# Kernel optimization log

Measured on AMD Instinct MI355X. Metric: run time of the kernel, lower is better.

The kernel has to match this reference:

```python
import jax, jax.numpy as jnp
import numpy as np

L, DIN, D, NL = 16384, 256, 768, 8
EPS = 1e-5


def _ln(x, g, b):
    mu = jnp.mean(x, axis=-1, keepdims=True)
    var = jnp.mean(jnp.square(x - mu), axis=-1, keepdims=True)
    return (x - mu) * jax.lax.rsqrt(var + EPS) * g + b


def setup_inputs() -> dict:
    key = jax.random.key(0)
    ks = iter(jax.random.split(key, 24))
    nrm = lambda shape, s=0.02: jax.random.normal(next(ks), shape, jnp.float32) * s
    return {
        "node_features": jax.random.normal(next(ks), (L, DIN), jnp.float32),
        "W_proj": nrm((DIN, D)), "b_proj": jnp.zeros((D,), jnp.float32),
        "ln_s_g": jnp.ones((NL, D), jnp.float32), "ln_s_b": jnp.zeros((NL, D), jnp.float32),
        "W_in": nrm((NL, D, D)), "b_in": jnp.zeros((NL, D), jnp.float32),
        "W_gate": nrm((NL, D, D)), "b_gate": jnp.zeros((NL, D), jnp.float32),
        "W_out": nrm((NL, D, D)), "b_out": jnp.zeros((NL, D), jnp.float32),
        "decay_logit": nrm((NL, D), 0.5),
        "ln_f_g": jnp.ones((NL, D), jnp.float32), "ln_f_b": jnp.zeros((NL, D), jnp.float32),
        "W_ff1": nrm((NL, D, 2 * D)), "b_ff1": jnp.zeros((NL, 2 * D), jnp.float32),
        "W_ff2": nrm((NL, 2 * D, D)), "b_ff2": jnp.zeros((NL, D), jnp.float32),
        "ln_o_g": jnp.ones((D,), jnp.float32), "ln_o_b": jnp.zeros((D,), jnp.float32),
    }


def reference(node_features, W_proj, b_proj, ln_s_g, ln_s_b, W_in, b_in,
              W_gate, b_gate, W_out, b_out, decay_logit, ln_f_g, ln_f_b,
              W_ff1, b_ff1, W_ff2, b_ff2, ln_o_g, ln_o_b):
    x = node_features @ W_proj + b_proj  # [L, D]
    for l in range(NL):
        h = _ln(x, ln_s_g[l], ln_s_b[l])
        u = h @ W_in[l] + b_in[l]                      # [L, D]
        gate = jax.nn.sigmoid(h @ W_gate[l] + b_gate[l])
        decay = jax.nn.sigmoid(decay_logit[l])         # [D]

        def step(state, u_t):
            state = decay * state + u_t
            return state, state

        _, states = jax.lax.scan(step, jnp.zeros((D,), x.dtype), u)  # [L, D]
        x = x + (states * gate) @ W_out[l] + b_out[l]
        hf = _ln(x, ln_f_g[l], ln_f_b[l])
        x = x + jax.nn.silu(hf @ W_ff1[l] + b_ff1[l]) @ W_ff2[l] + b_ff2[l]
    return _ln(x, ln_o_g, ln_o_b)
```

## Files before the change

### kernel.cpp

```cpp
#include <hip/hip_runtime.h>
#include <hip/hip_bf16.h>
#include <math.h>
#include <string.h>

#define L_TOK 16384
#define D_INP 256
#define D_MOD 768
#define D_FF  1536
#define N_LAYER 8
#define S_T 64
#define S_G 256
#define EPSV 1e-5f

typedef short bf16x8 __attribute__((ext_vector_type(8)));
typedef float f32x4 __attribute__((ext_vector_type(4)));
typedef __hip_bfloat16 bf16;
typedef unsigned int u32;
typedef unsigned short u16;

__device__ __forceinline__ float fsigmoid(float z) { return 1.0f / (1.0f + __expf(-z)); }

__device__ __forceinline__ u16 f2bf(float f) {
  __hip_bfloat16 h = __float2bfloat16(f);
  u16 r; memcpy(&r, &h, 2); return r;
}
__device__ __forceinline__ float bf2f(u16 v) {
  u32 x = ((u32)v) << 16; float f; memcpy(&f, &x, 4); return f;
}

__device__ __forceinline__ void glds16(const short* g, short* l) {
  __builtin_amdgcn_global_load_lds(
      (const __attribute__((address_space(1))) unsigned int*)(g),
      (__attribute__((address_space(3))) unsigned int*)(l), 16, 0, 0);
}

__global__ void k_f32_to_bf16v(const float4* __restrict__ src, ushort4* __restrict__ dst, int n4) {
  int i = blockIdx.x * blockDim.x + threadIdx.x;
  if (i < n4) {
    float4 v = src[i];
    ushort4 o; o.x = f2bf(v.x); o.y = f2bf(v.y); o.z = f2bf(v.z); o.w = f2bf(v.w);
    dst[i] = o;
  }
}

template<bool FOLD>
__global__ void k_transpose_fold(const float* __restrict__ src, bf16* __restrict__ dst,
                                 int R, int C, size_t sstride, size_t dstride,
                                 const float* __restrict__ gv, const float* __restrict__ bv,
                                 float* __restrict__ wacc, float* __restrict__ bacc,
                                 int vstride) {
  __shared__ float tile[32][33];
  int z = blockIdx.z;
  const float* s = src + (size_t)z * sstride;
  bf16* d = dst + (size_t)z * dstride;
  int r0 = blockIdx.y * 32, c0 = blockIdx.x * 32;
  int tx = threadIdx.x, ty = threadIdx.y;
#pragma unroll
  for (int i = ty; i < 32; i += 8)
    tile[i][tx] = s[(size_t)(r0 + i) * C + (c0 + tx)];
  __syncthreads();
  float gk = 1.0f;
  if (FOLD) gk = gv[(size_t)z * R + r0 + tx];
#pragma unroll
  for (int i = ty; i < 32; i += 8) {
    float val = tile[tx][i];
    if (FOLD) val *= gk;
    d[(size_t)(c0 + i) * R + (r0 + tx)] = __float2bfloat16(val);
  }
  if (FOLD && ty == 0) {
    const float* gz = gv + (size_t)z * R + r0;
    const float* bz = bv + (size_t)z * R + r0;
    float s1 = 0.f, s2 = 0.f;
#pragma unroll 8
    for (int j = 0; j < 32; j++) {
      float wv = tile[j][tx];
      s1 += gz[j] * wv;
      s2 += bz[j] * wv;
    }
    atomicAdd(&wacc[(size_t)z * vstride + c0 + tx], s1);
    atomicAdd(&bacc[(size_t)z * vstride + c0 + tx], s2);
  }
}

template<int MODE, bool LNFOLD, bool STATS>
__global__ __launch_bounds__(256, 4) void k_gemm128(
    const short* __restrict__ A, const short* __restrict__ Bt,
    const float* __restrict__ bias, const float* __restrict__ bias2,
    const float* __restrict__ wvec, const float* __restrict__ bvec,
    const float* __restrict__ stats_in, float* __restrict__ stats_out,
    u16* __restrict__ res, u16* __restrict__ outp, u16* __restrict__ outp2,
    int N, int K, int ncol)
{
  __shared__ short As[2][128 * 32];
  __shared__ short Bs[2][128 * 32];
  __shared__ float s_mu[128], s_rv[128];
  const int tid = threadIdx.x;
  const int lane = tid & 63, w = tid >> 6;
  const int wr = w >> 1, wc = w & 1;
  const int l16 = lane & 15, qd = lane >> 4;

  const int b = blockIdx.x;
  const int xcd = b & 7, t = b >> 3;
  const int m0 = (xcd * 16 + t / ncol) * 128;
  const int n0 = (t % ncol) * 128;

  const int sr = lane >> 2, sc = lane & 3;
  const int ar = w * 32 + sr;
  const int acx = sc ^ ((ar >> 1) & 3);
  const short* ag0 = A  + (size_t)(m0 + ar) * K + acx * 8;
  const short* ag1 = ag0 + (size_t)16 * K;
  const short* bg0 = Bt + (size_t)(n0 + ar) * K + acx * 8;
  const short* bg1 = bg0 + (size_t)16 * K;

  const int fo = (qd ^ ((l16 >> 1) & 3)) * 8 + l16 * 32;

  f32x4 acc[4][4];
#pragma unroll
  for (int i = 0; i < 4; i++)
#pragma unroll
    for (int j = 0; j < 4; j++) acc[i][j] = (f32x4){0.f, 0.f, 0.f, 0.f};

  {
    short* a0 = &As[0][w * 1024];
    glds16(ag0, a0); glds16(ag1, a0 + 512);
    short* b0 = &Bs[0][w * 1024];
    glds16(bg0, b0); glds16(bg1, b0 + 512);
  }
  if (LNFOLD && tid < 128) {
    float sv  = stats_in[2 * (m0 + tid)];
    float sq  = stats_in[2 * (m0 + tid) + 1];
    float mu  = sv * (1.0f / (float)D_MOD);
    float var = sq * (1.0f / (float)D_MOD) - mu * mu;
    s_mu[tid] = mu;
    s_rv[tid] = 1.0f / sqrtf(var + EPSV);
  }
  int p = 0;
  for (int k0 = 0; k0 < K; k0 += 32, p ^= 1) {
    __syncthreads();
    if (k0 + 32 < K) {
      short* a0 = &As[p ^ 1][w * 1024];
      glds16(ag0 + k0 + 32, a0); glds16(ag1 + k0 + 32, a0 + 512);
      short* b0 = &Bs[p ^ 1][w * 1024];
      glds16(bg0 + k0 + 32, b0); glds16(bg1 + k0 + 32, b0 + 512);
    }
    const short* afb = &As[p][wr * 2048 + fo];
    const short* bfb = &Bs[p][wc * 2048 + fo];
    bf16x8 af[4], bfr[4];
#pragma unroll
    for (int rt = 0; rt < 4; rt++) af[rt] = *(const bf16x8*)(afb + rt * 512);
#pragma unroll
    for (int ct = 0; ct < 4; ct++) bfr[ct] = *(const bf16x8*)(bfb + ct * 512);
#pragma unroll
    for (int rt = 0; rt < 4; rt++)
#pragma unroll
      for (int ct = 0; ct < 4; ct++)
        acc[rt][ct] = __builtin_amdgcn_mfma_f32_16x16x32_bf16(af[rt], bfr[ct], acc[rt][ct], 0, 0, 0);
  }

  const float* bb = bias;
  u16* op = outp;
  int nofs = 0, Nout = N;
  bool sig = false;
  if (MODE == 4) {
    Nout = N >> 1;
    if (n0 >= Nout) { bb = bias2; op = outp2; nofs = Nout; sig = true; }
  }
  const int gmb = m0 + wr * 64 + qd * 4;
  const int gnb = n0 + wc * 64 + l16;
  float bc[4], wv4[4], bv4[4];
#pragma unroll
  for (int ct = 0; ct < 4; ct++) {
    int gn = gnb + ct * 16;
    bc[ct] = bb[gn - nofs];
    if (LNFOLD) { wv4[ct] = wvec[gn]; bv4[ct] = bvec[gn]; }
  }
#pragma unroll
  for (int rt = 0; rt < 4; rt++) {
#pragma unroll
    for (int r = 0; r < 4; r++) {
      const int gm = gmb + rt * 16 + r;
      float mu = 0.f, rv = 0.f;
      if (LNFOLD) { mu = s_mu[gm - m0]; rv = s_rv[gm - m0]; }
      float ps = 0.f, ps2 = 0.f;
#pragma unroll
      for (int ct = 0; ct < 4; ct++) {
        int gn = gnb + ct * 16;
        float vv = acc[rt][ct][r];
        if (LNFOLD) vv = rv * vv - rv * mu * wv4[ct] + bv4[ct] + bc[ct];
        else        vv += bc[ct];
        if (MODE == 2) vv = vv * fsigmoid(vv);
        if (MODE == 4 && sig) vv = fsigmoid(vv);
        size_t oidx = (size_t)gm * Nout + (gn - nofs);
        if (MODE == 3) vv += bf2f(res[oidx]);
        u16 rb = f2bf(vv);
        op[oidx] = rb;
        if (STATS) { float fv = bf2f(rb); ps += fv; ps2 += fv * fv; }
      }
      if (STATS) {
#pragma unroll
        for (int o = 1; o < 16; o <<= 1) {
          ps  += __shfl_xor(ps, o, 64);
          ps2 += __shfl_xor(ps2, o, 64);
        }
        if (l16 == 0) {
          atomicAdd(&stats_out[2 * gm], ps);
          atomicAdd(&stats_out[2 * gm + 1], ps2);
        }
      }
    }
  }
}

__global__ void k_scan_a(const bf16* __restrict__ u, const float* __restrict__ dl,
                         float* __restrict__ clast) {
  int t = threadIdx.x;
  int g = blockIdx.x;
  int d0 = t * 4;
  float dec[4], s[4] = {0.f, 0.f, 0.f, 0.f};
#pragma unroll
  for (int c = 0; c < 4; c++) dec[c] = fsigmoid(dl[d0 + c]);
  const ushort4* up = (const ushort4*)(u + (size_t)g * S_T * D_MOD) + t;
  for (int tt = 0; tt < S_T; tt++) {
    ushort4 uv = up[(size_t)tt * 192];
    s[0] = fmaf(dec[0], s[0], bf2f(uv.x));
    s[1] = fmaf(dec[1], s[1], bf2f(uv.y));
    s[2] = fmaf(dec[2], s[2], bf2f(uv.z));
    s[3] = fmaf(dec[3], s[3], bf2f(uv.w));
  }
#pragma unroll
  for (int c = 0; c < 4; c++) clast[(size_t)g * D_MOD + d0 + c] = s[c];
}

__global__ void k_scan_b(const float* __restrict__ clast, const float* __restrict__ dl,
                         float* __restrict__ carry) {
  int d = threadIdx.x;
  float decay = fsigmoid(dl[d]);
  float aT = decay;
#pragma unroll
  for (int i = 0; i < 6; i++) aT *= aT;
  float c = 0.f;
  for (int g = 0; g < S_G; g++) {
    carry[(size_t)g * D_MOD + d] = c;
    c = fmaf(aT, c, clast[(size_t)g * D_MOD + d]);
  }
}

__global__ void k_scan_c(const bf16* __restrict__ u, const float* __restrict__ dl,
                         const float* __restrict__ carry, bf16* __restrict__ gate_s) {
  int t = threadIdx.x;
  int g = blockIdx.x;
  int d0 = t * 4;
  float dec[4], s[4];
#pragma unroll
  for (int c = 0; c < 4; c++) {
    dec[c] = fsigmoid(dl[d0 + c]);
    s[c] = carry[(size_t)g * D_MOD + d0 + c];
  }
  const ushort4* up = (const ushort4*)(u + (size_t)g * S_T * D_MOD) + t;
  ushort4* gp = (ushort4*)(gate_s + (size_t)g * S_T * D_MOD) + t;
  for (int tt = 0; tt < S_T; tt++) {
    ushort4 uv = up[(size_t)tt * 192];
    ushort4 gv = gp[(size_t)tt * 192];
    s[0] = fmaf(dec[0], s[0], bf2f(uv.x));
    s[1] = fmaf(dec[1], s[1], bf2f(uv.y));
    s[2] = fmaf(dec[2], s[2], bf2f(uv.z));
    s[3] = fmaf(dec[3], s[3], bf2f(uv.w));
    ushort4 ov;
    ov.x = f2bf(s[0] * bf2f(gv.x));
    ov.y = f2bf(s[1] * bf2f(gv.y));
    ov.z = f2bf(s[2] * bf2f(gv.z));
    ov.w = f2bf(s[3] * bf2f(gv.w));
    gp[(size_t)tt * 192] = ov;
  }
}

__global__ __launch_bounds__(256) void k_ln_final(const u16* __restrict__ x,
    const float* __restrict__ stats, const float* __restrict__ g,
    const float* __restrict__ b, float* __restrict__ outp) {
  int wv = threadIdx.x >> 6, lane = threadIdx.x & 63;
  int row = blockIdx.x * 4 + wv;
  float sv = stats[2 * row], sq = stats[2 * row + 1];
  float mu = sv * (1.0f / (float)D_MOD);
  float var = sq * (1.0f / (float)D_MOD) - mu * mu;
  float rv = 1.0f / sqrtf(var + EPSV);
  const ushort4* xr = (const ushort4*)(x + (size_t)row * D_MOD);
  const float4* g4 = (const float4*)g;
  const float4* b4 = (const float4*)b;
  float4* o4 = (float4*)(outp + (size_t)row * D_MOD);
#pragma unroll
  for (int j = 0; j < 3; j++) {
    int f = j * 64 + lane;
    ushort4 xv = xr[f];
    float4 gg = g4[f], bb = b4[f], ov;
    ov.x = (bf2f(xv.x) - mu) * rv * gg.x + bb.x;
    ov.y = (bf2f(xv.y) - mu) * rv * gg.y + bb.y;
    ov.z = (bf2f(xv.z) - mu) * rv * gg.z + bb.z;
    ov.w = (bf2f(xv.w) - mu) * rv * gg.w + bb.w;
    o4[f] = ov;
  }
}

extern "C" void kernel_launch(void* const* d_in, const int* in_sizes, int n_in,
                              void* d_out, int out_size, void* d_ws, size_t ws_size,
                              hipStream_t stream) {
  const float* nf     = (const float*)d_in[0];
  const float* W_proj = (const float*)d_in[1];
  const float* b_proj = (const float*)d_in[2];
  const float* ln_s_g = (const float*)d_in[3];
  const float* ln_s_b = (const float*)d_in[4];
  const float* W_in   = (const float*)d_in[5];
  const float* b_in   = (const float*)d_in[6];
  const float* W_gate = (const float*)d_in[7];
  const float* b_gate = (const float*)d_in[8];
  const float* W_out  = (const float*)d_in[9];
  const float* b_out  = (const float*)d_in[10];
  const float* dlogit = (const float*)d_in[11];
  const float* ln_f_g = (const float*)d_in[12];
  const float* ln_f_b = (const float*)d_in[13];
  const float* W_ff1  = (const float*)d_in[14];
  const float* b_ff1  = (const float*)d_in[15];
  const float* W_ff2  = (const float*)d_in[16];
  const float* b_ff2  = (const float*)d_in[17];
  const float* ln_o_g = (const float*)d_in[18];
  const float* ln_o_b = (const float*)d_in[19];
  (void)in_sizes; (void)n_in;

  char* ws = (char*)d_ws;
  size_t off = 0;
  auto alloc = [&](size_t bytes) -> char* {
    char* p = ws + off;
    off = (off + bytes + 255) & ~(size_t)255;
    return p;
  };
  const bool big = ws_size >= (160ull << 20);
  const size_t wmul = big ? N_LAYER : 1;

  u16*   x     = (u16*)alloc(2ull * L_TOK * D_MOD);
  char*  ug    = alloc(2ull * L_TOK * D_FF);
  u16*   u     = (u16*)ug;
  u16*   gate  = (u16*)(ug + 2ull * L_TOK * D_MOD);
  u16*   tb    = (u16*)ug;
  u16*   nfb   = (u16*)ug;
  bf16*  WprojT= (bf16*)alloc(2ull * D_INP * D_MOD);
  bf16*  WigT  = (bf16*)alloc(2ull * wmul * (2 * D_MOD) * D_MOD);
  bf16*  WoT   = (bf16*)alloc(2ull * wmul * D_MOD * D_MOD);
  bf16*  Wff1T = (bf16*)alloc(2ull * wmul * D_MOD * D_FF);
  bf16*  Wff2T = (bf16*)alloc(2ull * wmul * D_FF * D_MOD);
  float* clast = (float*)alloc(sizeof(float) * (size_t)S_G * D_MOD);
  float* carry = (float*)alloc(sizeof(float) * (size_t)S_G * D_MOD);
  char*  zbase = alloc(0);
  float* stats = (float*)alloc(sizeof(float) * 17ull * L_TOK * 2);
  float* wvig  = (float*)alloc(sizeof(float) * N_LAYER * 2 * D_MOD);
  float* bvig  = (float*)alloc(sizeof(float) * N_LAYER * 2 * D_MOD);
  float* wvf1  = (float*)alloc(sizeof(float) * N_LAYER * D_FF);
  float* bvf1  = (float*)alloc(sizeof(float) * N_LAYER * D_FF);
  size_t zbytes = (size_t)((char*)ws + off - zbase);
  hipMemsetAsync(zbase, 0, zbytes, stream);

  const size_t DD = (size_t)D_MOD * D_MOD, DF = (size_t)D_MOD * D_FF;
  auto statslot = [&](int s) { return stats + (size_t)s * L_TOK * 2; };
  dim3 tb32(32, 8);
  k_f32_to_bf16v<<<(L_TOK * D_INP / 4 + 255) / 256, 256, 0, stream>>>(
      (const float4*)nf, (ushort4*)nfb, L_TOK * D_INP / 4);
  k_transpose_fold<false><<<dim3(D_MOD / 32, D_INP / 32, 1), tb32, 0, stream>>>(
      W_proj, WprojT, D_INP, D_MOD, 0, 0, nullptr, nullptr, nullptr, nullptr, 0);
  if (big) {
    k_transpose_fold<true><<<dim3(D_MOD / 32, D_MOD / 32, N_LAYER), tb32, 0, stream>>>(
        W_in,   WigT,      D_MOD, D_MOD, DD, 2 * DD, ln_s_g, ln_s_b, wvig,       bvig,       2 * D_MOD);
    k_transpose_fold<true><<<dim3(D_MOD / 32, D_MOD / 32, N_LAYER), tb32, 0, stream>>>(
        W_gate, WigT + DD, D_MOD, D_MOD, DD, 2 * DD, ln_s_g, ln_s_b, wvig + D_MOD, bvig + D_MOD, 2 * D_MOD);
    k_transpose_fold<false><<<dim3(D_MOD / 32, D_MOD / 32, N_LAYER), tb32, 0, stream>>>(
        W_out,  WoT,       D_MOD, D_MOD, DD, DD, nullptr, nullptr, nullptr, nullptr, 0);
    k_transpose_fold<true><<<dim3(D_FF / 32,  D_MOD / 32, N_LAYER), tb32, 0, stream>>>(
        W_ff1,  Wff1T,     D_MOD, D_FF,  DF, DF, ln_f_g, ln_f_b, wvf1, bvf1, D_FF);
    k_transpose_fold<false><<<dim3(D_MOD / 32, D_FF / 32,  N_LAYER), tb32, 0, stream>>>(
        W_ff2,  Wff2T,     D_FF,  D_MOD, DF, DF, nullptr, nullptr, nullptr, nullptr, 0);
  }

  k_gemm128<0, false, true><<<128 * 6, 256, 0, stream>>>(
      (const short*)nfb, (const short*)WprojT, b_proj, nullptr, nullptr, nullptr,
      nullptr, statslot(0), nullptr, x, nullptr, D_MOD, D_INP, 6);

  for (int l = 0; l < N_LAYER; l++) {
    const bf16 *wigT, *woT, *wf1T, *wf2T;
    if (big) {
      wigT = WigT  + (size_t)l * 2 * DD;
      woT  = WoT   + (size_t)l * DD;
      wf1T = Wff1T + (size_t)l * DF;
      wf2T = Wff2T + (size_t)l * DF;
    } else {
      k_transpose_fold<true><<<dim3(D_MOD / 32, D_MOD / 32, 1), tb32, 0, stream>>>(
          W_in + (size_t)l * DD, WigT, D_MOD, D_MOD, 0, 0,
          ln_s_g + l * D_MOD, ln_s_b + l * D_MOD, wvig + (size_t)l * 2 * D_MOD, bvig + (size_t)l * 2 * D_MOD, 0);
      k_transpose_fold<true><<<dim3(D_MOD / 32, D_MOD / 32, 1), tb32, 0, stream>>>(
          W_gate + (size_t)l * DD, WigT + DD, D_MOD, D_MOD, 0, 0,
          ln_s_g + l * D_MOD, ln_s_b + l * D_MOD, wvig + (size_t)l * 2 * D_MOD + D_MOD, bvig + (size_t)l * 2 * D_MOD + D_MOD, 0);
      k_transpose_fold<false><<<dim3(D_MOD / 32, D_MOD / 32, 1), tb32, 0, stream>>>(
          W_out + (size_t)l * DD, WoT, D_MOD, D_MOD, 0, 0, nullptr, nullptr, nullptr, nullptr, 0);
      k_transpose_fold<true><<<dim3(D_FF / 32, D_MOD / 32, 1), tb32, 0, stream>>>(
          W_ff1 + (size_t)l * DF, Wff1T, D_MOD, D_FF, 0, 0,
          ln_f_g + l * D_MOD, ln_f_b + l * D_MOD, wvf1 + (size_t)l * D_FF, bvf1 + (size_t)l * D_FF, 0);
      k_transpose_fold<false><<<dim3(D_MOD / 32, D_FF / 32, 1), tb32, 0, stream>>>(
          W_ff2 + (size_t)l * DF, Wff2T, D_FF, D_MOD, 0, 0, nullptr, nullptr, nullptr, nullptr, 0);
      wigT = WigT; woT = WoT; wf1T = Wff1T; wf2T = Wff2T;
    }

    k_gemm128<4, true, false><<<128 * 12, 256, 0, stream>>>(
        (const short*)x, (const short*)wigT, b_in + l * D_MOD, b_gate + l * D_MOD,
        wvig + (size_t)l * 2 * D_MOD, bvig + (size_t)l * 2 * D_MOD,
        statslot(2 * l), nullptr, nullptr, u, gate, 2 * D_MOD, D_MOD, 12);
    k_scan_a<<<S_G, 192, 0, stream>>>((const bf16*)u, dlogit + l * D_MOD, clast);
    k_scan_b<<<1, D_MOD, 0, stream>>>(clast, dlogit + l * D_MOD, carry);
    k_scan_c<<<S_G, 192, 0, stream>>>((const bf16*)u, dlogit + l * D_MOD, carry, (bf16*)gate);
    k_gemm128<3, false, true><<<128 * 6, 256, 0, stream>>>(
        (const short*)gate, (const short*)woT, b_out + l * D_MOD, nullptr, nullptr, nullptr,
        nullptr, statslot(2 * l + 1), x, x, nullptr, D_MOD, D_MOD, 6);
    k_gemm128<2, true, false><<<128 * 12, 256, 0, stream>>>(
        (const short*)x, (const short*)wf1T, b_ff1 + l * D_FF, nullptr,
        wvf1 + (size_t)l * D_FF, bvf1 + (size_t)l * D_FF,
        statslot(2 * l + 1), nullptr, nullptr, tb, nullptr, D_FF, D_MOD, 12);
    k_gemm128<3, false, true><<<128 * 6, 256, 0, stream>>>(
        (const short*)tb, (const short*)wf2T, b_ff2 + l * D_MOD, nullptr, nullptr, nullptr,
        nullptr, statslot(2 * l + 2), x, x, nullptr, D_MOD, D_FF, 6);
  }

  k_ln_final<<<L_TOK / 4, 256, 0, stream>>>(x, statslot(2 * N_LAYER), ln_o_g, ln_o_b, (float*)d_out);
}
```

Before: 2.277 ms.

## Process two M-tiles per GEMM block, add 64-wide N tiles, fuse scan phases

The GEMM kernel now has each block compute two consecutive 128-row tiles, prefetching the second tile's first K-slice while the first is still computing. All GEMMs launch 768 blocks, so the grid fits in a single wave. The N=768 GEMMs switch to 128x64 tiles so their block count matches the wider ones. The scan's carry pass is folded into the first scan kernel through a last-block-done atomic counter, removing one launch. The trade-offs are a serialized tail in each block and a single-block carry pass that runs after all other scan blocks finish.

```diff
diff --git a/kernel.cpp b/kernel.cpp
--- a/kernel.cpp
+++ b/kernel.cpp
@@ -82,8 +82,8 @@
   }
 }
 
-template<int MODE, bool LNFOLD, bool STATS>
-__global__ __launch_bounds__(256, 4) void k_gemm128(
+template<int MODE, bool LNFOLD, bool STATS, int BN>
+__global__ __launch_bounds__(256, 4) void k_gemm(
     const short* __restrict__ A, const short* __restrict__ Bt,
     const float* __restrict__ bias, const float* __restrict__ bias2,
     const float* __restrict__ wvec, const float* __restrict__ bvec,
@@ -91,128 +91,169 @@
     u16* __restrict__ res, u16* __restrict__ outp, u16* __restrict__ outp2,
     int N, int K, int ncol)
 {
+  constexpr int CT = BN / 32;
   __shared__ short As[2][128 * 32];
-  __shared__ short Bs[2][128 * 32];
+  __shared__ short Bs[2][BN * 32];
   __shared__ float s_mu[128], s_rv[128];
   const int tid = threadIdx.x;
   const int lane = tid & 63, w = tid >> 6;
   const int wr = w >> 1, wc = w & 1;
   const int l16 = lane & 15, qd = lane >> 4;
 
-  const int b = blockIdx.x;
-  const int xcd = b & 7, t = b >> 3;
-  const int m0 = (xcd * 16 + t / ncol) * 128;
-  const int n0 = (t % ncol) * 128;
-
   const int sr = lane >> 2, sc = lane & 3;
   const int ar = w * 32 + sr;
-  const int acx = sc ^ ((ar >> 1) & 3);
-  const short* ag0 = A  + (size_t)(m0 + ar) * K + acx * 8;
-  const short* ag1 = ag0 + (size_t)16 * K;
-  const short* bg0 = Bt + (size_t)(n0 + ar) * K + acx * 8;
-  const short* bg1 = bg0 + (size_t)16 * K;
+  const int acxA = sc ^ ((ar >> 1) & 3);
+  const int bn64 = w * 16 + (lane >> 2);
+  const int acxB = sc ^ ((bn64 >> 1) & 3);
+
+  const int bid = blockIdx.x;
+  const int xcd = bid & 7, q = bid >> 3;
+  const int ccol = q % ncol, r2 = q / ncol;
+  const short *pA0[2], *pA1[2], *pB0[2], *pB1[2];
+  int pm0[2], pn0[2];
+#pragma unroll
+  for (int t = 0; t < 2; t++) {
+    int m0 = (xcd * 16 + r2 * 2 + t) * 128;
+    int n0 = ccol * BN;
+    pm0[t] = m0; pn0[t] = n0;
+    pA0[t] = A + (size_t)(m0 + ar) * K + acxA * 8;
+    pA1[t] = pA0[t] + (size_t)16 * K;
+    if (BN == 128) {
+      pB0[t] = Bt + (size_t)(n0 + ar) * K + acxA * 8;
+      pB1[t] = pB0[t] + (size_t)16 * K;
+    } else {
+      pB0[t] = Bt + (size_t)(n0 + bn64) * K + acxB * 8;
+      pB1[t] = nullptr;
+    }
+  }
+
+  auto issue = [&](int t, int ko, int st) {
+    short* al = &As[st][w * 1024];
+    glds16(pA0[t] + ko, al); glds16(pA1[t] + ko, al + 512);
+    if (BN == 128) {
+      short* bl = &Bs[st][w * 1024];
+      glds16(pB0[t] + ko, bl); glds16(pB1[t] + ko, bl + 512);
+    } else {
+      short* bl = &Bs[st][w * 512];
+      glds16(pB0[t] + ko, bl);
+    }
+  };
 
   const int fo = (qd ^ ((l16 >> 1) & 3)) * 8 + l16 * 32;
 
-  f32x4 acc[4][4];
+  f32x4 acc[4][CT];
 #pragma unroll
   for (int i = 0; i < 4; i++)
 #pragma unroll
-    for (int j = 0; j < 4; j++) acc[i][j] = (f32x4){0.f, 0.f, 0.f, 0.f};
-
-  {
-    short* a0 = &As[0][w * 1024];
-    glds16(ag0, a0); glds16(ag1, a0 + 512);
-    short* b0 = &Bs[0][w * 1024];
-    glds16(bg0, b0); glds16(bg1, b0 + 512);
-  }
+    for (int j = 0; j < CT; j++) acc[i][j] = (f32x4){0.f, 0.f, 0.f, 0.f};
+
+  issue(0, 0, 0);
   if (LNFOLD && tid < 128) {
-    float sv  = stats_in[2 * (m0 + tid)];
-    float sq  = stats_in[2 * (m0 + tid) + 1];
+    float sv  = stats_in[2 * (pm0[0] + tid)];
+    float sq  = stats_in[2 * (pm0[0] + tid) + 1];
     float mu  = sv * (1.0f / (float)D_MOD);
     float var = sq * (1.0f / (float)D_MOD) - mu * mu;
     s_mu[tid] = mu;
     s_rv[tid] = 1.0f / sqrtf(var + EPSV);
   }
+
+  const int NI = K >> 5;
   int p = 0;
-  for (int k0 = 0; k0 < K; k0 += 32, p ^= 1) {
-    __syncthreads();
-    if (k0 + 32 < K) {
-      short* a0 = &As[p ^ 1][w * 1024];
-      glds16(ag0 + k0 + 32, a0); glds16(ag1 + k0 + 32, a0 + 512);
-      short* b0 = &Bs[p ^ 1][w * 1024];
-      glds16(bg0 + k0 + 32, b0); glds16(bg1 + k0 + 32, b0 + 512);
-    }
-    const short* afb = &As[p][wr * 2048 + fo];
-    const short* bfb = &Bs[p][wc * 2048 + fo];
-    bf16x8 af[4], bfr[4];
-#pragma unroll
-    for (int rt = 0; rt < 4; rt++) af[rt] = *(const bf16x8*)(afb + rt * 512);
-#pragma unroll
-    for (int ct = 0; ct < 4; ct++) bfr[ct] = *(const bf16x8*)(bfb + ct * 512);
-#pragma unroll
-    for (int rt = 0; rt < 4; rt++)
-#pragma unroll
-      for (int ct = 0; ct < 4; ct++)
-        acc[rt][ct] = __builtin_amdgcn_mfma_f32_16x16x32_bf16(af[rt], bfr[ct], acc[rt][ct], 0, 0, 0);
-  }
-
-  const float* bb = bias;
-  u16* op = outp;
-  int nofs = 0, Nout = N;
-  bool sig = false;
-  if (MODE == 4) {
-    Nout = N >> 1;
-    if (n0 >= Nout) { bb = bias2; op = outp2; nofs = Nout; sig = true; }
-  }
-  const int gmb = m0 + wr * 64 + qd * 4;
-  const int gnb = n0 + wc * 64 + l16;
-  float bc[4], wv4[4], bv4[4];
-#pragma unroll
-  for (int ct = 0; ct < 4; ct++) {
-    int gn = gnb + ct * 16;
-    bc[ct] = bb[gn - nofs];
-    if (LNFOLD) { wv4[ct] = wvec[gn]; bv4[ct] = bvec[gn]; }
-  }
-#pragma unroll
-  for (int rt = 0; rt < 4; rt++) {
-#pragma unroll
-    for (int r = 0; r < 4; r++) {
-      const int gm = gmb + rt * 16 + r;
-      float mu = 0.f, rv = 0.f;
-      if (LNFOLD) { mu = s_mu[gm - m0]; rv = s_rv[gm - m0]; }
-      float ps = 0.f, ps2 = 0.f;
-#pragma unroll
-      for (int ct = 0; ct < 4; ct++) {
+  for (int t = 0; t < 2; t++) {
+    for (int i = 0; i < NI; i++) {
+      __syncthreads();
+      if (LNFOLD && t == 1 && i == 0 && tid < 128) {
+        float sv  = stats_in[2 * (pm0[1] + tid)];
+        float sq  = stats_in[2 * (pm0[1] + tid) + 1];
+        float mu  = sv * (1.0f / (float)D_MOD);
+        float var = sq * (1.0f / (float)D_MOD) - mu * mu;
+        s_mu[tid] = mu;
+        s_rv[tid] = 1.0f / sqrtf(var + EPSV);
+      }
+      if (i + 1 < NI)      issue(t, (i + 1) << 5, p ^ 1);
+      else if (t == 0)     issue(1, 0, p ^ 1);
+      const short* afb = &As[p][wr * 2048 + fo];
+      const short* bfb = &Bs[p][wc * (BN / 2) * 32 + fo];
+      bf16x8 af[4], bfr[CT];
+#pragma unroll
+      for (int rt = 0; rt < 4; rt++) af[rt] = *(const bf16x8*)(afb + rt * 512);
+#pragma unroll
+      for (int ct = 0; ct < CT; ct++) bfr[ct] = *(const bf16x8*)(bfb + ct * 512);
+#pragma unroll
+      for (int rt = 0; rt < 4; rt++)
+#pragma unroll
+        for (int ct = 0; ct < CT; ct++)
+          acc[rt][ct] = __builtin_amdgcn_mfma_f32_16x16x32_bf16(af[rt], bfr[ct], acc[rt][ct], 0, 0, 0);
+      p ^= 1;
+    }
+
+    {
+      const int m0 = pm0[t], n0 = pn0[t];
+      const float* bb = bias;
+      u16* op = outp;
+      int nofs = 0, Nout = N;
+      bool sig = false;
+      if (MODE == 4) {
+        Nout = N >> 1;
+        if (n0 >= Nout) { bb = bias2; op = outp2; nofs = Nout; sig = true; }
+      }
+      const int gmb = m0 + wr * 64 + qd * 4;
+      const int gnb = n0 + wc * (BN / 2) + l16;
+      float bc[CT], wv4[CT], bv4[CT];
+#pragma unroll
+      for (int ct = 0; ct < CT; ct++) {
         int gn = gnb + ct * 16;
-        float vv = acc[rt][ct][r];
-        if (LNFOLD) vv = rv * vv - rv * mu * wv4[ct] + bv4[ct] + bc[ct];
-        else        vv += bc[ct];
-        if (MODE == 2) vv = vv * fsigmoid(vv);
-        if (MODE == 4 && sig) vv = fsigmoid(vv);
-        size_t oidx = (size_t)gm * Nout + (gn - nofs);
-        if (MODE == 3) vv += bf2f(res[oidx]);
-        u16 rb = f2bf(vv);
-        op[oidx] = rb;
-        if (STATS) { float fv = bf2f(rb); ps += fv; ps2 += fv * fv; }
+        bc[ct] = bb[gn - nofs];
+        if (LNFOLD) { wv4[ct] = wvec[gn]; bv4[ct] = bvec[gn]; }
       }
-      if (STATS) {
-#pragma unroll
-        for (int o = 1; o < 16; o <<= 1) {
-          ps  += __shfl_xor(ps, o, 64);
-          ps2 += __shfl_xor(ps2, o, 64);
-        }
-        if (l16 == 0) {
-          atomicAdd(&stats_out[2 * gm], ps);
-          atomicAdd(&stats_out[2 * gm + 1], ps2);
+#pragma unroll
+      for (int rt = 0; rt < 4; rt++) {
+#pragma unroll
+        for (int r = 0; r < 4; r++) {
+          const int gm = gmb + rt * 16 + r;
+          float mu = 0.f, rv = 0.f;
+          if (LNFOLD) { mu = s_mu[gm - m0]; rv = s_rv[gm - m0]; }
+          float ps = 0.f, ps2 = 0.f;
+#pragma unroll
+          for (int ct = 0; ct < CT; ct++) {
+            int gn = gnb + ct * 16;
+            float vv = acc[rt][ct][r];
+            if (LNFOLD) vv = rv * vv - rv * mu * wv4[ct] + bv4[ct] + bc[ct];
+            else        vv += bc[ct];
+            if (MODE == 2) vv = vv * fsigmoid(vv);
+            if (MODE == 4 && sig) vv = fsigmoid(vv);
+            size_t oidx = (size_t)gm * Nout + (gn - nofs);
+            if (MODE == 3) vv += bf2f(res[oidx]);
+            u16 rb = f2bf(vv);
+            op[oidx] = rb;
+            if (STATS) { float fv = bf2f(rb); ps += fv; ps2 += fv * fv; }
+          }
+          if (STATS) {
+#pragma unroll
+            for (int o = 1; o < 16; o <<= 1) {
+              ps  += __shfl_xor(ps, o, 64);
+              ps2 += __shfl_xor(ps2, o, 64);
+            }
+            if (l16 == 0) {
+              atomicAdd(&stats_out[2 * gm], ps);
+              atomicAdd(&stats_out[2 * gm + 1], ps2);
+            }
+          }
         }
       }
     }
-  }
-}
-
-__global__ void k_scan_a(const bf16* __restrict__ u, const float* __restrict__ dl,
-                         float* __restrict__ clast) {
+    if (t == 0) {
+#pragma unroll
+      for (int i = 0; i < 4; i++)
+#pragma unroll
+        for (int j = 0; j < CT; j++) acc[i][j] = (f32x4){0.f, 0.f, 0.f, 0.f};
+    }
+  }
+}
+
+__global__ void k_scan_ab(const bf16* __restrict__ u, const float* __restrict__ dl,
+                          float* __restrict__ clast, float* __restrict__ carry,
+                          unsigned int* __restrict__ counter) {
   int t = threadIdx.x;
   int g = blockIdx.x;
   int d0 = t * 4;
@@ -228,20 +269,35 @@
     s[3] = fmaf(dec[3], s[3], bf2f(uv.w));
   }
 #pragma unroll
-  for (int c = 0; c < 4; c++) clast[(size_t)g * D_MOD + d0 + c] = s[c];
-}
-
-__global__ void k_scan_b(const float* __restrict__ clast, const float* __restrict__ dl,
-                         float* __restrict__ carry) {
-  int d = threadIdx.x;
-  float decay = fsigmoid(dl[d]);
-  float aT = decay;
-#pragma unroll
-  for (int i = 0; i < 6; i++) aT *= aT;
-  float c = 0.f;
-  for (int g = 0; g < S_G; g++) {
-    carry[(size_t)g * D_MOD + d] = c;
-    c = fmaf(aT, c, clast[(size_t)g * D_MOD + d]);
+  for (int c = 0; c < 4; c++)
+    __hip_atomic_store(&clast[(size_t)g * D_MOD + d0 + c], s[c],
+                       __ATOMIC_RELAXED, __HIP_MEMORY_SCOPE_AGENT);
+  __threadfence();
+  __shared__ int lastf;
+  __syncthreads();
+  if (t == 0) lastf = (atomicAdd(counter, 1) == S_G - 1) ? 1 : 0;
+  __syncthreads();
+  if (!lastf) return;
+  if (t == 0) *counter = 0;
+  __threadfence();
+  float aT[4];
+#pragma unroll
+  for (int c = 0; c < 4; c++) {
+    float dd = dec[c];
+#pragma unroll
+    for (int i = 0; i < 6; i++) dd *= dd;
+    aT[c] = dd;
+  }
+  float cc[4] = {0.f, 0.f, 0.f, 0.f};
+  for (int g2 = 0; g2 < S_G; g2++) {
+    size_t base = (size_t)g2 * D_MOD + d0;
+#pragma unroll
+    for (int c = 0; c < 4; c++) carry[base + c] = cc[c];
+#pragma unroll
+    for (int c = 0; c < 4; c++) {
+      float v = __hip_atomic_load(&clast[base + c], __ATOMIC_RELAXED, __HIP_MEMORY_SCOPE_AGENT);
+      cc[c] = fmaf(aT[c], cc[c], v);
+    }
   }
 }
 
@@ -354,6 +410,7 @@
   float* bvig  = (float*)alloc(sizeof(float) * N_LAYER * 2 * D_MOD);
   float* wvf1  = (float*)alloc(sizeof(float) * N_LAYER * D_FF);
   float* bvf1  = (float*)alloc(sizeof(float) * N_LAYER * D_FF);
+  unsigned int* scnt = (unsigned int*)alloc(sizeof(unsigned int) * 16);
   size_t zbytes = (size_t)((char*)ws + off - zbase);
   hipMemsetAsync(zbase, 0, zbytes, stream);
 
@@ -366,7 +423,7 @@
       W_proj, WprojT, D_INP, D_MOD, 0, 0, nullptr, nullptr, nullptr, nullptr, 0);
   if (big) {
     k_transpose_fold<true><<<dim3(D_MOD / 32, D_MOD / 32, N_LAYER), tb32, 0, stream>>>(
-        W_in,   WigT,      D_MOD, D_MOD, DD, 2 * DD, ln_s_g, ln_s_b, wvig,       bvig,       2 * D_MOD);
+        W_in,   WigT,      D_MOD, D_MOD, DD, 2 * DD, ln_s_g, ln_s_b, wvig,         bvig,         2 * D_MOD);
     k_transpose_fold<true><<<dim3(D_MOD / 32, D_MOD / 32, N_LAYER), tb32, 0, stream>>>(
         W_gate, WigT + DD, D_MOD, D_MOD, DD, 2 * DD, ln_s_g, ln_s_b, wvig + D_MOD, bvig + D_MOD, 2 * D_MOD);
     k_transpose_fold<false><<<dim3(D_MOD / 32, D_MOD / 32, N_LAYER), tb32, 0, stream>>>(
@@ -377,9 +434,9 @@
         W_ff2,  Wff2T,     D_FF,  D_MOD, DF, DF, nullptr, nullptr, nullptr, nullptr, 0);
   }
 
-  k_gemm128<0, false, true><<<128 * 6, 256, 0, stream>>>(
+  k_gemm<0, false, true, 64><<<768, 256, 0, stream>>>(
       (const short*)nfb, (const short*)WprojT, b_proj, nullptr, nullptr, nullptr,
-      nullptr, statslot(0), nullptr, x, nullptr, D_MOD, D_INP, 6);
+      nullptr, statslot(0), nullptr, x, nullptr, D_MOD, D_INP, 12);
 
   for (int l = 0; l < N_LAYER; l++) {
     const bf16 *wigT, *woT, *wf1T, *wf2T;
@@ -405,23 +462,22 @@
       wigT = WigT; woT = WoT; wf1T = Wff1T; wf2T = Wff2T;
     }
 
-    k_gemm128<4, true, false><<<128 * 12, 256, 0, stream>>>(
+    k_gemm<4, true, false, 128><<<768, 256, 0, stream>>>(
         (const short*)x, (const short*)wigT, b_in + l * D_MOD, b_gate + l * D_MOD,
         wvig + (size_t)l * 2 * D_MOD, bvig + (size_t)l * 2 * D_MOD,
         statslot(2 * l), nullptr, nullptr, u, gate, 2 * D_MOD, D_MOD, 12);
-    k_scan_a<<<S_G, 192, 0, stream>>>((const bf16*)u, dlogit + l * D_MOD, clast);
-    k_scan_b<<<1, D_MOD, 0, stream>>>(clast, dlogit + l * D_MOD, carry);
+    k_scan_ab<<<S_G, 192, 0, stream>>>((const bf16*)u, dlogit + l * D_MOD, clast, carry, scnt);
     k_scan_c<<<S_G, 192, 0, stream>>>((const bf16*)u, dlogit + l * D_MOD, carry, (bf16*)gate);
-    k_gemm128<3, false, true><<<128 * 6, 256, 0, stream>>>(
+    k_gemm<3, false, true, 64><<<768, 256, 0, stream>>>(
         (const short*)gate, (const short*)woT, b_out + l * D_MOD, nullptr, nullptr, nullptr,
-        nullptr, statslot(2 * l + 1), x, x, nullptr, D_MOD, D_MOD, 6);
-    k_gemm128<2, true, false><<<128 * 12, 256, 0, stream>>>(
+        nullptr, statslot(2 * l + 1), x, x, nullptr, D_MOD, D_MOD, 12);
+    k_gemm<2, true, false, 128><<<768, 256, 0, stream>>>(
         (const short*)x, (const short*)wf1T, b_ff1 + l * D_FF, nullptr,
         wvf1 + (size_t)l * D_FF, bvf1 + (size_t)l * D_FF,
         statslot(2 * l + 1), nullptr, nullptr, tb, nullptr, D_FF, D_MOD, 12);
-    k_gemm128<3, false, true><<<128 * 6, 256, 0, stream>>>(
+    k_gemm<3, false, true, 64><<<768, 256, 0, stream>>>(
         (const short*)tb, (const short*)wf2T, b_ff2 + l * D_MOD, nullptr, nullptr, nullptr,
-        nullptr, statslot(2 * l + 2), x, x, nullptr, D_MOD, D_FF, 6);
+        nullptr, statslot(2 * l + 2), x, x, nullptr, D_MOD, D_FF, 12);
   }
 
   k_ln_final<<<L_TOK / 4, 256, 0, stream>>>(x, statslot(2 * N_LAYER), ln_o_g, ln_o_b, (float*)d_out);
```

New measurement: 4.796 ms. +110.6%, slower.
